# Kernel optimization log

Hardware: AMD Instinct MI355X
Metric: run time of the kernel (lower is better)

## Reference

```python
import jax, jax.numpy as jnp
import numpy as np

V, H, E, L = 50257, 1024, 1024, 2048


def setup_inputs() -> dict:
    key = jax.random.key(0)
    ks = jax.random.split(key, 13)
    s = 0.05
    return {
        'y_i': jax.random.randint(ks[0], (1, 1), 0, V),
        'h_i': jax.random.normal(ks[1], (1, 1, H), jnp.float32),
        'cnn_a': jax.random.normal(ks[2], (1, H, L), jnp.float32),
        'cnn_c': jax.random.normal(ks[3], (1, H, L), jnp.float32),
        'emb': jax.random.normal(ks[4], (V, H), jnp.float32) * s,
        'W_t': jax.random.normal(ks[5], (E, H), jnp.float32) * s,
        'b_t': jax.random.normal(ks[6], (E,), jnp.float32) * s,
        'W_ih': jax.random.normal(ks[7], (3 * H, H + E), jnp.float32) * s,
        'W_hh': jax.random.normal(ks[8], (3 * H, H), jnp.float32) * s,
        'b_ih': jax.random.normal(ks[9], (3 * H,), jnp.float32) * s,
        'b_hh': jax.random.normal(ks[10], (3 * H,), jnp.float32) * s,
        'W_o': jax.random.normal(ks[11], (V, H), jnp.float32) * s,
        'b_o': jax.random.normal(ks[12], (V,), jnp.float32) * s,
    }


def reference(y_i, h_i, cnn_a, cnn_c, emb, W_t, b_t, W_ih, W_hh, b_ih, b_hh, W_o, b_o):
    # g_i = embedding(y_i); dropout is identity in eval mode
    g = emb[y_i]                                   # [1,1,H]
    # d_i = Linear(h_i) + g_i
    d = h_i @ W_t.T + b_t + g                      # [1,1,E]
    # attention: softmax(bmm(d_i, cnn_a))
    scores = jnp.einsum('bte,bel->btl', d, cnn_a).reshape(1, -1)  # [1,L]
    a = jax.nn.softmax(scores, axis=-1)
    # c_i = bmm(a, cnn_c^T)
    c = jnp.einsum('btl,bhl->bth', a.reshape(1, 1, -1), cnn_c)    # [1,1,H]
    # single-step, single-layer GRU (PyTorch gate order: r, z, n)
    x = jnp.concatenate((g, c), axis=-1)[0]        # [1, H+E]
    h0 = h_i[0]                                    # [1, H]
    gx = x @ W_ih.T + b_ih                         # [1, 3H]
    gh = h0 @ W_hh.T + b_hh                        # [1, 3H]
    r = jax.nn.sigmoid(gx[:, :H] + gh[:, :H])
    z = jax.nn.sigmoid(gx[:, H:2 * H] + gh[:, H:2 * H])
    n = jnp.tanh(gx[:, 2 * H:] + r * gh[:, 2 * H:])
    h_new = (1.0 - z) * n + z * h0                 # [1, H]
    gru_hidden = h_new[None]                       # [1,1,H]
    # output distribution
    logits = h_new @ W_o.T + b_o                   # [1, V]
    softmax_output = jax.nn.log_softmax(logits, axis=-1)
    return (softmax_output, gru_hidden)
```

## Files before the change

kernel.cpp:

```cpp
#include <hip/hip_runtime.h>
#include <math.h>

#define Hn 1024
#define En 1024
#define Ln 2048
#define Vn 50257

__device__ __forceinline__ float waveReduceSum(float v) {
#pragma unroll
    for (int off = 32; off > 0; off >>= 1)
        v += __shfl_down(v, off, 64);
    return v;
}

__device__ __forceinline__ float waveReduceMax(float v) {
#pragma unroll
    for (int off = 32; off > 0; off >>= 1)
        v = fmaxf(v, __shfl_down(v, off, 64));
    return v;
}

__global__ void k_d(const float* __restrict__ h_i, const float* __restrict__ W_t,
                    const float* __restrict__ b_t, const float* __restrict__ emb,
                    const int* __restrict__ y, float* __restrict__ d) {
    __shared__ float red[4];
    const int t = threadIdx.x;
    const int e = blockIdx.x;
    const float4 w = ((const float4*)(W_t + (size_t)e * Hn))[t];
    const float4 h = ((const float4*)h_i)[t];
    float acc = w.x * h.x + w.y * h.y + w.z * h.z + w.w * h.w;
    acc = waveReduceSum(acc);
    if ((t & 63) == 0) red[t >> 6] = acc;
    __syncthreads();
    if (t == 0) {
        float s = red[0] + red[1] + red[2] + red[3];
        d[e] = s + b_t[e] + emb[(size_t)y[0] * Hn + e];
    }
}

__global__ void k_scores(const float* __restrict__ d, const float* __restrict__ cnn_a,
                         float* __restrict__ part) {
    __shared__ float dsh[64];
    const int t = threadIdx.x;
    const int e0 = blockIdx.y * 64;
    if (t < 64) dsh[t] = d[e0 + t];
    __syncthreads();
    const int l = blockIdx.x * 256 + t;
    float acc = 0.f;
#pragma unroll 8
    for (int e = 0; e < 64; ++e)
        acc += dsh[e] * cnn_a[(size_t)(e0 + e) * Ln + l];
    part[(size_t)blockIdx.y * Ln + l] = acc;
}

__global__ void k_softmax(const float* __restrict__ part, float* __restrict__ a) {
    __shared__ float red[16];
    __shared__ float m_s, s_s;
    const int t = threadIdx.x;
    float v0 = 0.f, v1 = 0.f;
#pragma unroll
    for (int p = 0; p < 16; ++p) {
        v0 += part[(size_t)p * Ln + t];
        v1 += part[(size_t)p * Ln + t + 1024];
    }
    float m = fmaxf(v0, v1);
    m = waveReduceMax(m);
    if ((t & 63) == 0) red[t >> 6] = m;
    __syncthreads();
    if (t == 0) {
        float mm = red[0];
#pragma unroll
        for (int i = 1; i < 16; ++i) mm = fmaxf(mm, red[i]);
        m_s = mm;
    }
    __syncthreads();
    m = m_s;
    const float e0 = expf(v0 - m), e1 = expf(v1 - m);
    float s = e0 + e1;
    s = waveReduceSum(s);
    if ((t & 63) == 0) red[t >> 6] = s;
    __syncthreads();
    if (t == 0) {
        float ss = 0.f;
#pragma unroll
        for (int i = 0; i < 16; ++i) ss += red[i];
        s_s = ss;
    }
    __syncthreads();
    const float inv = 1.0f / s_s;
    a[t] = e0 * inv;
    a[t + 1024] = e1 * inv;
}

__global__ void k_c(const float* __restrict__ a, const float* __restrict__ cnn_c,
                    float* __restrict__ c) {
    __shared__ float red[4];
    const int t = threadIdx.x;
    const int h = blockIdx.x;
    const float4* r4 = (const float4*)(cnn_c + (size_t)h * Ln);
    const float4* a4 = (const float4*)a;
    float acc = 0.f;
#pragma unroll
    for (int j = 0; j < 2; ++j) {
        const int idx = t + j * 256;
        const float4 w = r4[idx];
        const float4 av = a4[idx];
        acc += w.x * av.x + w.y * av.y + w.z * av.z + w.w * av.w;
    }
    acc = waveReduceSum(acc);
    if ((t & 63) == 0) red[t >> 6] = acc;
    __syncthreads();
    if (t == 0) c[h] = red[0] + red[1] + red[2] + red[3];
}

__global__ void k_gru(const float* __restrict__ emb, const int* __restrict__ y,
                      const float* __restrict__ c, const float* __restrict__ h0,
                      const float* __restrict__ W_ih, const float* __restrict__ W_hh,
                      const float* __restrict__ b_ih, const float* __restrict__ b_hh,
                      float* __restrict__ gx, float* __restrict__ gh) {
    __shared__ float redx[4], redh[4];
    const int t = threadIdx.x;
    const int i = blockIdx.x;
    const float* g = emb + (size_t)y[0] * Hn;
    const float4* wih = (const float4*)(W_ih + (size_t)i * (Hn + En));
    const float4* whh = (const float4*)(W_hh + (size_t)i * Hn);
    float accx, acch;
    {
        float4 w = wih[t];
        float4 xv = ((const float4*)g)[t];
        accx = w.x * xv.x + w.y * xv.y + w.z * xv.z + w.w * xv.w;
        w = wih[t + 256];
        xv = ((const float4*)c)[t];
        accx += w.x * xv.x + w.y * xv.y + w.z * xv.z + w.w * xv.w;
    }
    {
        const float4 w = whh[t];
        const float4 hv = ((const float4*)h0)[t];
        acch = w.x * hv.x + w.y * hv.y + w.z * hv.z + w.w * hv.w;
    }
    accx = waveReduceSum(accx);
    acch = waveReduceSum(acch);
    if ((t & 63) == 0) { redx[t >> 6] = accx; redh[t >> 6] = acch; }
    __syncthreads();
    if (t == 0) {
        gx[i] = redx[0] + redx[1] + redx[2] + redx[3] + b_ih[i];
        gh[i] = redh[0] + redh[1] + redh[2] + redh[3] + b_hh[i];
    }
}

__global__ void k_gates(const float* __restrict__ gx, const float* __restrict__ gh,
                        const float* __restrict__ h0, float* __restrict__ hn,
                        float* __restrict__ out_h) {
    const int i = blockIdx.x * 256 + threadIdx.x;
    const float r = 1.f / (1.f + expf(-(gx[i] + gh[i])));
    const float z = 1.f / (1.f + expf(-(gx[Hn + i] + gh[Hn + i])));
    const float n = tanhf(gx[2 * Hn + i] + r * gh[2 * Hn + i]);
    const float hv = (1.f - z) * n + z * h0[i];
    hn[i] = hv;
    out_h[i] = hv;
}

__global__ __launch_bounds__(256) void k_logits(const float* __restrict__ W_o,
                                                const float* __restrict__ b_o,
                                                const float* __restrict__ hn,
                                                float* __restrict__ logits) {
    __shared__ float hsh[Hn];
    const int t = threadIdx.x;
    ((float4*)hsh)[t] = ((const float4*)hn)[t];
    __syncthreads();
    const int wid = t >> 6, lane = t & 63;
    const int v = blockIdx.x * 4 + wid;
    if (v >= Vn) return;
    const float4* row = (const float4*)(W_o + (size_t)v * Hn);
    const float4* h4 = (const float4*)hsh;
    float acc = 0.f;
#pragma unroll
    for (int j = 0; j < 4; ++j) {
        const float4 w = row[lane + j * 64];
        const float4 hv = h4[lane + j * 64];
        acc += w.x * hv.x + w.y * hv.y + w.z * hv.z + w.w * hv.w;
    }
    acc = waveReduceSum(acc);
    if (lane == 0) logits[v] = acc + b_o[v];
}

__global__ void k_logsoftmax(float* __restrict__ out) {
    __shared__ float red[16];
    __shared__ float m_s, s_s;
    const int t = threadIdx.x;
    float m = -INFINITY;
    for (int v = t; v < Vn; v += 1024) m = fmaxf(m, out[v]);
    m = waveReduceMax(m);
    if ((t & 63) == 0) red[t >> 6] = m;
    __syncthreads();
    if (t == 0) {
        float mm = red[0];
#pragma unroll
        for (int i = 1; i < 16; ++i) mm = fmaxf(mm, red[i]);
        m_s = mm;
    }
    __syncthreads();
    m = m_s;
    float s = 0.f;
    for (int v = t; v < Vn; v += 1024) s += expf(out[v] - m);
    s = waveReduceSum(s);
    if ((t & 63) == 0) red[t >> 6] = s;
    __syncthreads();
    if (t == 0) {
        float ss = 0.f;
#pragma unroll
        for (int i = 0; i < 16; ++i) ss += red[i];
        s_s = ss;
    }
    __syncthreads();
    const float lse = m + logf(s_s);
    for (int v = t; v < Vn; v += 1024) out[v] = out[v] - lse;
}

extern "C" void kernel_launch(void* const* d_in, const int* in_sizes, int n_in,
                              void* d_out, int out_size, void* d_ws, size_t ws_size,
                              hipStream_t stream) {
    const int*   y     = (const int*)d_in[0];
    const float* h_i   = (const float*)d_in[1];
    const float* cnn_a = (const float*)d_in[2];
    const float* cnn_c = (const float*)d_in[3];
    const float* emb   = (const float*)d_in[4];
    const float* W_t   = (const float*)d_in[5];
    const float* b_t   = (const float*)d_in[6];
    const float* W_ih  = (const float*)d_in[7];
    const float* W_hh  = (const float*)d_in[8];
    const float* b_ih  = (const float*)d_in[9];
    const float* b_hh  = (const float*)d_in[10];
    const float* W_o   = (const float*)d_in[11];
    const float* b_o   = (const float*)d_in[12];
    float* out = (float*)d_out;

    float* ws    = (float*)d_ws;
    float* d_vec = ws;
    float* part  = d_vec + 1024;
    float* a_vec = part + 16 * Ln;
    float* c_vec = a_vec + Ln;
    float* gx    = c_vec + Hn;
    float* gh    = gx + 3 * Hn;
    float* hn    = gh + 3 * Hn;

    k_d<<<dim3(En), dim3(256), 0, stream>>>(h_i, W_t, b_t, emb, y, d_vec);
    k_scores<<<dim3(8, 16), dim3(256), 0, stream>>>(d_vec, cnn_a, part);
    k_softmax<<<dim3(1), dim3(1024), 0, stream>>>(part, a_vec);
    k_c<<<dim3(Hn), dim3(256), 0, stream>>>(a_vec, cnn_c, c_vec);
    k_gru<<<dim3(3 * Hn), dim3(256), 0, stream>>>(emb, y, c_vec, h_i, W_ih, W_hh,
                                                  b_ih, b_hh, gx, gh);
    k_gates<<<dim3(4), dim3(256), 0, stream>>>(gx, gh, h_i, hn, out + Vn);
    k_logits<<<dim3((Vn + 3) / 4), dim3(256), 0, stream>>>(W_o, b_o, hn, out);
    k_logsoftmax<<<dim3(1), dim3(1024), 0, stream>>>(out);
}
```

Baseline: 448.3 us.

## Fuse attention, softmax-context and GRU stages into fewer kernels

```diff
diff --git a/kernel.cpp b/kernel.cpp
--- a/kernel.cpp
+++ b/kernel.cpp
@@ -20,30 +20,34 @@
     return v;
 }
 
-__global__ void k_d(const float* __restrict__ h_i, const float* __restrict__ W_t,
-                    const float* __restrict__ b_t, const float* __restrict__ emb,
-                    const int* __restrict__ y, float* __restrict__ d) {
-    __shared__ float red[4];
-    const int t = threadIdx.x;
-    const int e = blockIdx.x;
-    const float4 w = ((const float4*)(W_t + (size_t)e * Hn))[t];
-    const float4 h = ((const float4*)h_i)[t];
-    float acc = w.x * h.x + w.y * h.y + w.z * h.z + w.w * h.w;
-    acc = waveReduceSum(acc);
-    if ((t & 63) == 0) red[t >> 6] = acc;
-    __syncthreads();
-    if (t == 0) {
-        float s = red[0] + red[1] + red[2] + red[3];
-        d[e] = s + b_t[e] + emb[(size_t)y[0] * Hn + e];
-    }
-}
-
-__global__ void k_scores(const float* __restrict__ d, const float* __restrict__ cnn_a,
-                         float* __restrict__ part) {
+__global__ __launch_bounds__(256) void k_d_scores(
+    const float* __restrict__ h_i, const float* __restrict__ W_t,
+    const float* __restrict__ b_t, const float* __restrict__ emb,
+    const int* __restrict__ y, const float* __restrict__ cnn_a,
+    float* __restrict__ part) {
     __shared__ float dsh[64];
-    const int t = threadIdx.x;
+    const int t = threadIdx.x, wave = t >> 6, lane = t & 63;
     const int e0 = blockIdx.y * 64;
-    if (t < 64) dsh[t] = d[e0 + t];
+    const float4* h4 = (const float4*)h_i;
+    float4 hfrag[4];
+#pragma unroll
+    for (int k = 0; k < 4; ++k) hfrag[k] = h4[lane + k * 64];
+    const int yy = y[0];
+#pragma unroll 4
+    for (int rr = 0; rr < 16; ++rr) {
+        const int row = wave * 16 + rr;
+        const float4* wrow = (const float4*)(W_t + (size_t)(e0 + row) * Hn);
+        float acc = 0.f;
+#pragma unroll
+        for (int k = 0; k < 4; ++k) {
+            const float4 w = wrow[lane + k * 64];
+            acc += w.x * hfrag[k].x + w.y * hfrag[k].y +
+                   w.z * hfrag[k].z + w.w * hfrag[k].w;
+        }
+        acc = waveReduceSum(acc);
+        if (lane == 0)
+            dsh[row] = acc + b_t[e0 + row] + emb[(size_t)yy * Hn + e0 + row];
+    }
     __syncthreads();
     const int l = blockIdx.x * 256 + t;
     float acc = 0.f;
@@ -53,123 +57,109 @@
     part[(size_t)blockIdx.y * Ln + l] = acc;
 }
 
-__global__ void k_softmax(const float* __restrict__ part, float* __restrict__ a) {
-    __shared__ float red[16];
-    __shared__ float m_s, s_s;
-    const int t = threadIdx.x;
-    float v0 = 0.f, v1 = 0.f;
+__global__ __launch_bounds__(256) void k_softmax_c(
+    const float* __restrict__ part, const float* __restrict__ cnn_c,
+    float* __restrict__ c) {
+    __shared__ float red[4];
+    __shared__ float bc;
+    const int t = threadIdx.x, wave = t >> 6, lane = t & 63;
+    const int h = blockIdx.x;
+    const float4* p4 = (const float4*)part;
+    float4 r0 = {0.f, 0.f, 0.f, 0.f}, r1 = {0.f, 0.f, 0.f, 0.f};
 #pragma unroll
     for (int p = 0; p < 16; ++p) {
-        v0 += part[(size_t)p * Ln + t];
-        v1 += part[(size_t)p * Ln + t + 1024];
-    }
-    float m = fmaxf(v0, v1);
+        const float4 a = p4[p * 512 + t];
+        const float4 b = p4[p * 512 + 256 + t];
+        r0.x += a.x; r0.y += a.y; r0.z += a.z; r0.w += a.w;
+        r1.x += b.x; r1.y += b.y; r1.z += b.z; r1.w += b.w;
+    }
+    float m = fmaxf(fmaxf(fmaxf(r0.x, r0.y), fmaxf(r0.z, r0.w)),
+                    fmaxf(fmaxf(r1.x, r1.y), fmaxf(r1.z, r1.w)));
     m = waveReduceMax(m);
-    if ((t & 63) == 0) red[t >> 6] = m;
-    __syncthreads();
-    if (t == 0) {
-        float mm = red[0];
-#pragma unroll
-        for (int i = 1; i < 16; ++i) mm = fmaxf(mm, red[i]);
-        m_s = mm;
-    }
-    __syncthreads();
-    m = m_s;
-    const float e0 = expf(v0 - m), e1 = expf(v1 - m);
-    float s = e0 + e1;
+    if (lane == 0) red[wave] = m;
+    __syncthreads();
+    if (t == 0) bc = fmaxf(fmaxf(red[0], red[1]), fmaxf(red[2], red[3]));
+    __syncthreads();
+    const float M = bc;
+    const float e0 = expf(r0.x - M), e1 = expf(r0.y - M);
+    const float e2 = expf(r0.z - M), e3 = expf(r0.w - M);
+    const float e4 = expf(r1.x - M), e5 = expf(r1.y - M);
+    const float e6 = expf(r1.z - M), e7 = expf(r1.w - M);
+    float s = e0 + e1 + e2 + e3 + e4 + e5 + e6 + e7;
     s = waveReduceSum(s);
-    if ((t & 63) == 0) red[t >> 6] = s;
-    __syncthreads();
-    if (t == 0) {
-        float ss = 0.f;
-#pragma unroll
-        for (int i = 0; i < 16; ++i) ss += red[i];
-        s_s = ss;
-    }
-    __syncthreads();
-    const float inv = 1.0f / s_s;
-    a[t] = e0 * inv;
-    a[t + 1024] = e1 * inv;
-}
-
-__global__ void k_c(const float* __restrict__ a, const float* __restrict__ cnn_c,
-                    float* __restrict__ c) {
-    __shared__ float red[4];
-    const int t = threadIdx.x;
-    const int h = blockIdx.x;
-    const float4* r4 = (const float4*)(cnn_c + (size_t)h * Ln);
-    const float4* a4 = (const float4*)a;
-    float acc = 0.f;
-#pragma unroll
-    for (int j = 0; j < 2; ++j) {
-        const int idx = t + j * 256;
-        const float4 w = r4[idx];
-        const float4 av = a4[idx];
-        acc += w.x * av.x + w.y * av.y + w.z * av.z + w.w * av.w;
-    }
-    acc = waveReduceSum(acc);
-    if ((t & 63) == 0) red[t >> 6] = acc;
-    __syncthreads();
-    if (t == 0) c[h] = red[0] + red[1] + red[2] + red[3];
-}
-
-__global__ void k_gru(const float* __restrict__ emb, const int* __restrict__ y,
-                      const float* __restrict__ c, const float* __restrict__ h0,
-                      const float* __restrict__ W_ih, const float* __restrict__ W_hh,
-                      const float* __restrict__ b_ih, const float* __restrict__ b_hh,
-                      float* __restrict__ gx, float* __restrict__ gh) {
-    __shared__ float redx[4], redh[4];
-    const int t = threadIdx.x;
+    if (lane == 0) red[wave] = s;
+    __syncthreads();
+    if (t == 0) bc = red[0] + red[1] + red[2] + red[3];
+    __syncthreads();
+    const float inv = 1.0f / bc;
+    const float4* crow = (const float4*)(cnn_c + (size_t)h * Ln);
+    const float4 w0 = crow[t], w1 = crow[t + 256];
+    float pc = e0 * w0.x + e1 * w0.y + e2 * w0.z + e3 * w0.w +
+               e4 * w1.x + e5 * w1.y + e6 * w1.z + e7 * w1.w;
+    pc = waveReduceSum(pc);
+    if (lane == 0) red[wave] = pc;
+    __syncthreads();
+    if (t == 0) c[h] = (red[0] + red[1] + red[2] + red[3]) * inv;
+}
+
+__global__ __launch_bounds__(256) void k_gru_fused(
+    const float* __restrict__ emb, const int* __restrict__ y,
+    const float* __restrict__ c, const float* __restrict__ h0,
+    const float* __restrict__ W_ih, const float* __restrict__ W_hh,
+    const float* __restrict__ b_ih, const float* __restrict__ b_hh,
+    float* __restrict__ out_h) {
+    __shared__ float redx[3][4], redh[3][4];
+    const int t = threadIdx.x, wave = t >> 6, lane = t & 63;
     const int i = blockIdx.x;
     const float* g = emb + (size_t)y[0] * Hn;
-    const float4* wih = (const float4*)(W_ih + (size_t)i * (Hn + En));
-    const float4* whh = (const float4*)(W_hh + (size_t)i * Hn);
-    float accx, acch;
-    {
-        float4 w = wih[t];
-        float4 xv = ((const float4*)g)[t];
-        accx = w.x * xv.x + w.y * xv.y + w.z * xv.z + w.w * xv.w;
-        w = wih[t + 256];
-        xv = ((const float4*)c)[t];
-        accx += w.x * xv.x + w.y * xv.y + w.z * xv.z + w.w * xv.w;
-    }
-    {
-        const float4 w = whh[t];
-        const float4 hv = ((const float4*)h0)[t];
-        acch = w.x * hv.x + w.y * hv.y + w.z * hv.z + w.w * hv.w;
-    }
-    accx = waveReduceSum(accx);
-    acch = waveReduceSum(acch);
-    if ((t & 63) == 0) { redx[t >> 6] = accx; redh[t >> 6] = acch; }
+    const float4 gv = ((const float4*)g)[t];
+    const float4 cv = ((const float4*)c)[t];
+    const float4 hv = ((const float4*)h0)[t];
+    float ax[3], ah[3];
+#pragma unroll
+    for (int j = 0; j < 3; ++j) {
+        const float4* wih = (const float4*)(W_ih + (size_t)(j * Hn + i) * (Hn + En));
+        const float4 w0 = wih[t];
+        const float4 w1 = wih[t + 256];
+        ax[j] = w0.x * gv.x + w0.y * gv.y + w0.z * gv.z + w0.w * gv.w +
+                w1.x * cv.x + w1.y * cv.y + w1.z * cv.z + w1.w * cv.w;
+        const float4* whh = (const float4*)(W_hh + (size_t)(j * Hn + i) * Hn);
+        const float4 w2 = whh[t];
+        ah[j] = w2.x * hv.x + w2.y * hv.y + w2.z * hv.z + w2.w * hv.w;
+    }
+#pragma unroll
+    for (int j = 0; j < 3; ++j) {
+        ax[j] = waveReduceSum(ax[j]);
+        ah[j] = waveReduceSum(ah[j]);
+    }
+    if (lane == 0) {
+#pragma unroll
+        for (int j = 0; j < 3; ++j) { redx[j][wave] = ax[j]; redh[j][wave] = ah[j]; }
+    }
     __syncthreads();
     if (t == 0) {
-        gx[i] = redx[0] + redx[1] + redx[2] + redx[3] + b_ih[i];
-        gh[i] = redh[0] + redh[1] + redh[2] + redh[3] + b_hh[i];
-    }
-}
-
-__global__ void k_gates(const float* __restrict__ gx, const float* __restrict__ gh,
-                        const float* __restrict__ h0, float* __restrict__ hn,
-                        float* __restrict__ out_h) {
-    const int i = blockIdx.x * 256 + threadIdx.x;
-    const float r = 1.f / (1.f + expf(-(gx[i] + gh[i])));
-    const float z = 1.f / (1.f + expf(-(gx[Hn + i] + gh[Hn + i])));
-    const float n = tanhf(gx[2 * Hn + i] + r * gh[2 * Hn + i]);
-    const float hv = (1.f - z) * n + z * h0[i];
-    hn[i] = hv;
-    out_h[i] = hv;
-}
-
-__global__ __launch_bounds__(256) void k_logits(const float* __restrict__ W_o,
-                                                const float* __restrict__ b_o,
-                                                const float* __restrict__ hn,
-                                                float* __restrict__ logits) {
+        float gx[3], gh[3];
+#pragma unroll
+        for (int j = 0; j < 3; ++j) {
+            gx[j] = redx[j][0] + redx[j][1] + redx[j][2] + redx[j][3] + b_ih[j * Hn + i];
+            gh[j] = redh[j][0] + redh[j][1] + redh[j][2] + redh[j][3] + b_hh[j * Hn + i];
+        }
+        const float r = 1.f / (1.f + expf(-(gx[0] + gh[0])));
+        const float z = 1.f / (1.f + expf(-(gx[1] + gh[1])));
+        const float n = tanhf(gx[2] + r * gh[2]);
+        out_h[i] = (1.f - z) * n + z * h0[i];
+    }
+}
+
+__global__ __launch_bounds__(1024) void k_logits(
+    const float* __restrict__ W_o, const float* __restrict__ b_o,
+    const float* __restrict__ hn, float* __restrict__ logits) {
     __shared__ float hsh[Hn];
     const int t = threadIdx.x;
-    ((float4*)hsh)[t] = ((const float4*)hn)[t];
+    if (t < 256) ((float4*)hsh)[t] = ((const float4*)hn)[t];
     __syncthreads();
     const int wid = t >> 6, lane = t & 63;
-    const int v = blockIdx.x * 4 + wid;
+    const int v = blockIdx.x * 16 + wid;
     if (v >= Vn) return;
     const float4* row = (const float4*)(W_o + (size_t)v * Hn);
     const float4* h4 = (const float4*)hsh;
@@ -184,12 +174,18 @@
     if (lane == 0) logits[v] = acc + b_o[v];
 }
 
-__global__ void k_logsoftmax(float* __restrict__ out) {
+__global__ __launch_bounds__(1024) void k_logsoftmax(float* __restrict__ out) {
     __shared__ float red[16];
-    __shared__ float m_s, s_s;
+    __shared__ float bc;
     const int t = threadIdx.x;
+    float4* o4 = (float4*)out;
+    const int N4 = Vn / 4;
     float m = -INFINITY;
-    for (int v = t; v < Vn; v += 1024) m = fmaxf(m, out[v]);
+    for (int i = t; i < N4; i += 1024) {
+        const float4 v = o4[i];
+        m = fmaxf(m, fmaxf(fmaxf(v.x, v.y), fmaxf(v.z, v.w)));
+    }
+    if (t == 0) m = fmaxf(m, out[Vn - 1]);
     m = waveReduceMax(m);
     if ((t & 63) == 0) red[t >> 6] = m;
     __syncthreads();
@@ -197,12 +193,16 @@
         float mm = red[0];
 #pragma unroll
         for (int i = 1; i < 16; ++i) mm = fmaxf(mm, red[i]);
-        m_s = mm;
-    }
-    __syncthreads();
-    m = m_s;
+        bc = mm;
+    }
+    __syncthreads();
+    const float M = bc;
     float s = 0.f;
-    for (int v = t; v < Vn; v += 1024) s += expf(out[v] - m);
+    for (int i = t; i < N4; i += 1024) {
+        const float4 v = o4[i];
+        s += expf(v.x - M) + expf(v.y - M) + expf(v.z - M) + expf(v.w - M);
+    }
+    if (t == 0) s += expf(out[Vn - 1] - M);
     s = waveReduceSum(s);
     if ((t & 63) == 0) red[t >> 6] = s;
     __syncthreads();
@@ -210,11 +210,16 @@
         float ss = 0.f;
 #pragma unroll
         for (int i = 0; i < 16; ++i) ss += red[i];
-        s_s = ss;
-    }
-    __syncthreads();
-    const float lse = m + logf(s_s);
-    for (int v = t; v < Vn; v += 1024) out[v] = out[v] - lse;
+        bc = M + logf(ss);
+    }
+    __syncthreads();
+    const float lse = bc;
+    for (int i = t; i < N4; i += 1024) {
+        float4 v = o4[i];
+        v.x -= lse; v.y -= lse; v.z -= lse; v.w -= lse;
+        o4[i] = v;
+    }
+    if (t == 0) out[Vn - 1] -= lse;
 }
 
 extern "C" void kernel_launch(void* const* d_in, const int* in_sizes, int n_in,
@@ -236,21 +241,16 @@
     float* out = (float*)d_out;
 
     float* ws    = (float*)d_ws;
-    float* d_vec = ws;
-    float* part  = d_vec + 1024;
-    float* a_vec = part + 16 * Ln;
-    float* c_vec = a_vec + Ln;
-    float* gx    = c_vec + Hn;
-    float* gh    = gx + 3 * Hn;
-    float* hn    = gh + 3 * Hn;
-
-    k_d<<<dim3(En), dim3(256), 0, stream>>>(h_i, W_t, b_t, emb, y, d_vec);
-    k_scores<<<dim3(8, 16), dim3(256), 0, stream>>>(d_vec, cnn_a, part);
-    k_softmax<<<dim3(1), dim3(1024), 0, stream>>>(part, a_vec);
-    k_c<<<dim3(Hn), dim3(256), 0, stream>>>(a_vec, cnn_c, c_vec);
-    k_gru<<<dim3(3 * Hn), dim3(256), 0, stream>>>(emb, y, c_vec, h_i, W_ih, W_hh,
-                                                  b_ih, b_hh, gx, gh);
-    k_gates<<<dim3(4), dim3(256), 0, stream>>>(gx, gh, h_i, hn, out + Vn);
-    k_logits<<<dim3((Vn + 3) / 4), dim3(256), 0, stream>>>(W_o, b_o, hn, out);
+    float* part  = ws;
+    float* c_vec = part + 16 * Ln;
+
+    float* out_h = out + Vn;
+
+    k_d_scores<<<dim3(8, 16), dim3(256), 0, stream>>>(h_i, W_t, b_t, emb, y,
+                                                      cnn_a, part);
+    k_softmax_c<<<dim3(Hn), dim3(256), 0, stream>>>(part, cnn_c, c_vec);
+    k_gru_fused<<<dim3(Hn), dim3(256), 0, stream>>>(emb, y, c_vec, h_i, W_ih,
+                                                    W_hh, b_ih, b_hh, out_h);
+    k_logits<<<dim3((Vn + 15) / 16), dim3(1024), 0, stream>>>(W_o, b_o, out_h, out);
     k_logsoftmax<<<dim3(1), dim3(1024), 0, stream>>>(out);
 }
```

Result: slower. 458.6 us (+2.3%).
